# Kernel optimization log

Measured on AMD Instinct MI355X. Metric: run time of the kernel, lower is better.

The kernel has to match this reference:

```python
import jax, jax.numpy as jnp
import numpy as np

N_NODES = 100000
N_EDGES = 3200000  # avg degree 32
IN_FEATS = 512
N_HIDDEN = 128
N_CLASSES = 64
K = 10  # n_layers of gated APPNP propagation


def setup_inputs() -> dict:
    key = jax.random.key(0)
    ks = jax.random.split(key, 6)
    features = jax.random.normal(ks[0], (N_NODES, IN_FEATS), dtype=jnp.float32)
    W1 = jax.random.normal(ks[1], (IN_FEATS, N_HIDDEN), dtype=jnp.float32) * (1.0 / np.sqrt(IN_FEATS))
    b1 = jnp.zeros((N_HIDDEN,), jnp.float32)
    W2 = jax.random.normal(ks[2], (N_HIDDEN, N_CLASSES), dtype=jnp.float32) * (1.0 / np.sqrt(N_HIDDEN))
    b2 = jnp.zeros((N_CLASSES,), jnp.float32)
    init_weight_y = jax.random.normal(ks[3], (IN_FEATS, N_CLASSES), dtype=jnp.float32) * (1.0 / np.sqrt(IN_FEATS))
    edge_index = jax.random.randint(ks[4], (2, N_EDGES), 0, N_NODES, dtype=jnp.int32)
    return {
        "features": features, "W1": W1, "b1": b1, "W2": W2, "b2": b2,
        "init_weight_y": init_weight_y, "edge_index": edge_index,
    }


def reference(features, W1, b1, W2, b2, init_weight_y, edge_index):
    # Eval-mode forward: feat/edge dropout are identity.
    src, dst = edge_index[0], edge_index[1]
    n = features.shape[0]
    # Symmetric GCN normalization D^{-1/2} A D^{-1/2} from in-degrees.
    deg = jax.ops.segment_sum(jnp.ones(src.shape, features.dtype), dst, num_segments=n)
    norm = jax.lax.rsqrt(jnp.clip(deg, 1.0))
    ew = (norm[src] * norm[dst])[:, None]  # [E,1] edge weights

    def spmm(x):  # A_hat @ x via gather-multiply-scatter
        return jax.ops.segment_sum(x[src] * ew, dst, num_segments=n)

    # feature transform: dropout(identity) -> linear -> relu
    h = jax.nn.relu(features @ W1 + b1)                      # [N,H]
    logits = jax.nn.softmax(features @ init_weight_y, axis=1)  # [N,C]
    # project predictions before propagation (APPNP propagates class scores)
    h0 = h @ W2 + b2                                         # [N,C]

    def step(carry, _):
        hc, lg = carry
        agg_lg = spmm(lg)                                    # neighbor soft labels
        # gate: per-node agreement between own and aggregated soft labels
        z = jax.nn.sigmoid(jnp.sum(lg * agg_lg, axis=1, keepdims=True))  # [N,1]
        h_new = z * spmm(hc) + (1.0 - z) * h0                # gated APPNP hop
        return (h_new, agg_lg), None

    (h_out, _), _ = jax.lax.scan(step, (h0, logits), None, length=K)
    return h_out
```

## Files before the change

### kernel.cpp

```cpp
#include <hip/hip_runtime.h>

typedef __attribute__((ext_vector_type(8))) short bf16x8;
typedef __attribute__((ext_vector_type(4))) short bf16x4;
typedef __attribute__((ext_vector_type(4))) float f32x4;
typedef __attribute__((ext_vector_type(4))) unsigned int u32x4;

__device__ __forceinline__ unsigned short f2bf(float f) {
  unsigned int u = __float_as_uint(f);
  u += 0x7fffu + ((u >> 16) & 1u);
  return (unsigned short)(u >> 16);
}
__device__ __forceinline__ float bflo(unsigned int w) { return __uint_as_float(w << 16); }
__device__ __forceinline__ float bfhi(unsigned int w) { return __uint_as_float(w & 0xffff0000u); }

__device__ __forceinline__ short* ldsp(short* base, int row, int rowbytes, int colshort) {
  int off = row * rowbytes + colshort * 2;
  off ^= ((row & 7) << 4);
  return (short*)((char*)base + off);
}

#define CHUNK 8192
#define NBMAX 512

__global__ __launch_bounds__(256) void k_bhist(const int* __restrict__ ei, int E, int NB,
                                               int* __restrict__ gcnt, int* __restrict__ wghist) {
  __shared__ int h[NBMAX];
  for (int t = threadIdx.x; t < NB; t += 256) h[t] = 0;
  __syncthreads();
  int base = blockIdx.x * CHUNK;
#pragma unroll
  for (int i = 0; i < CHUNK / 256; ++i) {
    int e = base + i * 256 + threadIdx.x;
    if (e < E) atomicAdd(&h[ei[E + e] >> 8], 1);
  }
  __syncthreads();
  for (int t = threadIdx.x; t < NB; t += 256) {
    int c = h[t];
    wghist[blockIdx.x * NBMAX + t] = c;
    if (c) atomicAdd(&gcnt[t], c);
  }
}

__global__ void k_bscan(const int* __restrict__ gcnt, int* __restrict__ bbase,
                        int* __restrict__ gcur, int* __restrict__ offs, int NB, int N) {
  __shared__ int sm[512];
  int t = threadIdx.x;
  int v = (t < NB) ? gcnt[t] : 0;
  sm[t] = v;
  __syncthreads();
  for (int o = 1; o < 512; o <<= 1) {
    int x = (t >= o) ? sm[t - o] : 0;
    __syncthreads();
    sm[t] += x;
    __syncthreads();
  }
  if (t < NB) { int e = sm[t] - v; bbase[t] = e; gcur[t] = e; }
  if (t == 511) { bbase[NB] = sm[511]; offs[N] = sm[511]; }
}

__global__ __launch_bounds__(256) void k_bucket(const int* __restrict__ ei,
                                                const int* __restrict__ wghist,
                                                int* __restrict__ gcur,
                                                int2* __restrict__ bpairs, int E, int NB) {
  __shared__ int lbase[NBMAX];
  __shared__ int lcur[NBMAX];
  for (int t = threadIdx.x; t < NB; t += 256) {
    int c = wghist[blockIdx.x * NBMAX + t];
    lbase[t] = c ? atomicAdd(&gcur[t], c) : 0;
    lcur[t] = 0;
  }
  __syncthreads();
  int base = blockIdx.x * CHUNK;
#pragma unroll
  for (int i = 0; i < CHUNK / 256; ++i) {
    int e = base + i * 256 + threadIdx.x;
    if (e < E) {
      int s = ei[e], d = ei[E + e];
      int b = d >> 8;
      int p = lbase[b] + atomicAdd(&lcur[b], 1);
      bpairs[p] = make_int2(s, d);
    }
  }
}

__global__ __launch_bounds__(256) void k_csr(const int2* __restrict__ bpairs,
                                             const int* __restrict__ bbase,
                                             int* __restrict__ offs, float* __restrict__ nrm,
                                             int* __restrict__ csr_src,
                                             int* __restrict__ gslots, int N) {
  __shared__ int hist[256];
  __shared__ int scan[256];
  __shared__ int cur[256];
  const int t = threadIdx.x;
  const int b = blockIdx.x;
  const int d0 = b << 8;
  const int nn = min(256, N - d0);
  const int base = bbase[b], end = bbase[b + 1];
  hist[t] = 0;
  __syncthreads();
  for (int e = base + t; e < end; e += 256) atomicAdd(&hist[bpairs[e].y - d0], 1);
  __syncthreads();
  int myc = hist[t];
  scan[t] = myc;
  __syncthreads();
  for (int o = 1; o < 256; o <<= 1) {
    int x = (t >= o) ? scan[t - o] : 0;
    __syncthreads();
    scan[t] += x;
    __syncthreads();
  }
  int excl = scan[t] - myc;
  if (t < nn) {
    offs[d0 + t] = base + excl;
    nrm[d0 + t] = rsqrtf(fmaxf((float)myc, 1.f));
  }
  if (t < 64) {
    int w0 = hist[4 * t + 0], w1 = hist[4 * t + 1];
    int w2 = hist[4 * t + 2], w3 = hist[4 * t + 3];
    gslots[b * 64 + t] = 4 * max(max(w0, w1), max(w2, w3));
  }
  cur[t] = excl;
  __syncthreads();
  for (int e = base + t; e < end; e += 256) {
    int2 pr = bpairs[e];
    int pos = atomicAdd(&cur[pr.y - d0], 1);
    csr_src[base + pos] = pr.x;
  }
}

__global__ void k_scan1(const int* __restrict__ in, int* __restrict__ out,
                        int* __restrict__ bsum, int n) {
  __shared__ int sm[1024];
  int t = threadIdx.x;
  int gid = blockIdx.x * 1024 + t;
  int v = (gid < n) ? in[gid] : 0;
  sm[t] = v;
  __syncthreads();
  for (int off = 1; off < 1024; off <<= 1) {
    int x = (t >= off) ? sm[t - off] : 0;
    __syncthreads();
    sm[t] += x;
    __syncthreads();
  }
  if (gid < n) out[gid] = sm[t] - v;
  if (t == 1023) bsum[blockIdx.x] = sm[1023];
}

__global__ void k_scan2(int* __restrict__ bsum, int nb) {
  __shared__ int sm[128];
  int t = threadIdx.x;
  int v = (t < nb) ? bsum[t] : 0;
  sm[t] = v;
  __syncthreads();
  for (int o = 1; o < 128; o <<= 1) {
    int x = (t >= o) ? sm[t - o] : 0;
    __syncthreads();
    sm[t] += x;
    __syncthreads();
  }
  if (t < nb) bsum[t] = sm[t] - v;
  if (t == 127) bsum[nb] = sm[127];
}

__global__ void k_scan3(int* __restrict__ out, const int* __restrict__ bsum, int n) {
  int gid = blockIdx.x * 1024 + threadIdx.x;
  if (gid < n) out[gid] += bsum[blockIdx.x];
  if (gid == 0) out[n] = bsum[gridDim.x];
}

__global__ __launch_bounds__(64) void k_ell(
    const int* __restrict__ offs, const int* __restrict__ csr_src,
    const int* __restrict__ gof, unsigned* __restrict__ pidx,
    unsigned int* __restrict__ pkA, unsigned int* __restrict__ pkB, int N) {
  int g = blockIdx.x;
  int t = threadIdx.x;
  if (g == 0) {
    pkA[(size_t)N * 64 + t] = 0;
    pkB[(size_t)N * 64 + t] = 0;
  }
  int base = gof[g];
  int slots = gof[g + 1] - base;
  int o[4], d[4];
#pragma unroll
  for (int s = 0; s < 4; ++s) {
    int nd_ = g * 4 + s;
    o[s] = (nd_ < N) ? offs[nd_] : 0;
    d[s] = (nd_ < N) ? (offs[nd_ + 1] - o[s]) : 0;
  }
  unsigned zoff = (unsigned)N << 8;
  for (int j = t; j < slots; j += 64) {
    int i = j >> 2, s = j & 3;
    pidx[base + j] = (i < d[s]) ? ((unsigned)csr_src[o[s] + i] << 8) : zoff;
  }
}

__global__ void k_wprep(const float* __restrict__ W1, const float* __restrict__ Wy,
                        unsigned short* __restrict__ Wt) {
  int k = blockIdx.x, j = threadIdx.x;
  float v = (j < 128) ? W1[k * 128 + j] : Wy[k * 64 + (j - 128)];
  Wt[j * 512 + k] = f2bf(v);
}
__global__ void k_wprep2(const float* __restrict__ W2, unsigned short* __restrict__ Wt2) {
  int k = blockIdx.x, j = threadIdx.x;
  Wt2[j * 128 + k] = f2bf(W2[k * 64 + j]);
}

__global__ __launch_bounds__(256) void k_transform(
    const unsigned short* __restrict__ Wt, const unsigned short* __restrict__ Wt2,
    const float* __restrict__ X, const float* __restrict__ b1, const float* __restrict__ b2,
    const float* __restrict__ nrm,
    unsigned int* __restrict__ pk0, unsigned short* __restrict__ h0b, int n)
{
  __shared__ short Xs[128 * 32];
  __shared__ short Ws[192 * 32];
  __shared__ short Hs[128 * 128];
  __shared__ short W2s[64 * 128];

  const int tid = threadIdx.x;
  const int w = tid >> 6;
  const int lane = tid & 63;
  const int c = lane & 15;
  const int g = lane >> 4;
  const int m0 = blockIdx.x * 128;

#pragma unroll
  for (int i = 0; i < 4; ++i) {
    int cc = tid + i * 256;
    int j2 = cc >> 4, k8 = (cc & 15) * 8;
    bf16x8 v = *(const bf16x8*)&Wt2[j2 * 128 + k8];
    *(bf16x8*)ldsp(W2s, j2, 256, k8) = v;
  }

  f32x4 zero4 = {0.f, 0.f, 0.f, 0.f};
  f32x4 acc[2][12];
#pragma unroll
  for (int mi = 0; mi < 2; ++mi)
#pragma unroll
    for (int i = 0; i < 12; ++i) acc[mi][i] = zero4;

  const int xr = tid >> 1;
  const int xc = (tid & 1) * 16;
  const int xrow = m0 + xr;

  for (int kk = 0; kk < 512; kk += 32) {
    float4 f[4];
    if (xrow < n) {
      const float4* p = (const float4*)(X + (size_t)xrow * 512 + kk + xc);
      f[0] = p[0]; f[1] = p[1]; f[2] = p[2]; f[3] = p[3];
    } else {
      float4 z = {0.f, 0.f, 0.f, 0.f};
      f[0] = z; f[1] = z; f[2] = z; f[3] = z;
    }
    bf16x8 lo, hi;
    {
      const float* fp = (const float*)f;
#pragma unroll
      for (int q = 0; q < 8; ++q) { lo[q] = (short)f2bf(fp[q]); hi[q] = (short)f2bf(fp[8 + q]); }
    }
    *(bf16x8*)ldsp(Xs, xr, 64, xc) = lo;
    *(bf16x8*)ldsp(Xs, xr, 64, xc + 8) = hi;
#pragma unroll
    for (int i = 0; i < 3; ++i) {
      int cc = tid + i * 256;
      int j = cc >> 2, k8 = (cc & 3) * 8;
      bf16x8 v = *(const bf16x8*)&Wt[j * 512 + kk + k8];
      *(bf16x8*)ldsp(Ws, j, 64, k8) = v;
    }
    __syncthreads();
    bf16x8 bx0 = *(const bf16x8*)ldsp(Xs, w * 32 + c, 64, g * 8);
    bf16x8 bx1 = *(const bf16x8*)ldsp(Xs, w * 32 + 16 + c, 64, g * 8);
#pragma unroll
    for (int jt = 0; jt < 12; ++jt) {
      bf16x8 aw = *(const bf16x8*)ldsp(Ws, jt * 16 + c, 64, g * 8);
      acc[0][jt] = __builtin_amdgcn_mfma_f32_16x16x32_bf16(aw, bx0, acc[0][jt], 0, 0, 0);
      acc[1][jt] = __builtin_amdgcn_mfma_f32_16x16x32_bf16(aw, bx1, acc[1][jt], 0, 0, 0);
    }
    __syncthreads();
  }

  float lv[2][16];
  float inv_[2];
#pragma unroll
  for (int mi = 0; mi < 2; ++mi) {
    int m = w * 32 + mi * 16 + c;
#pragma unroll
    for (int jt = 0; jt < 8; ++jt) {
      int jb = jt * 16 + g * 4;
      bf16x4 hv;
#pragma unroll
      for (int q = 0; q < 4; ++q) {
        float hvf = fmaxf(acc[mi][jt][q] + b1[jb + q], 0.f);
        hv[q] = (short)f2bf(hvf);
      }
      *(bf16x4*)ldsp(Hs, m, 256, jb) = hv;
    }
    float mx = -3.4e38f;
#pragma unroll
    for (int t = 0; t < 4; ++t)
#pragma unroll
      for (int q = 0; q < 4; ++q) {
        float vv = acc[mi][8 + t][q];
        lv[mi][t * 4 + q] = vv;
        mx = fmaxf(mx, vv);
      }
    mx = fmaxf(mx, __shfl_xor(mx, 16, 64));
    mx = fmaxf(mx, __shfl_xor(mx, 32, 64));
    float sum = 0.f;
#pragma unroll
    for (int i = 0; i < 16; ++i) { lv[mi][i] = __expf(lv[mi][i] - mx); sum += lv[mi][i]; }
    sum += __shfl_xor(sum, 16, 64);
    sum += __shfl_xor(sum, 32, 64);
    inv_[mi] = 1.f / sum;
  }
  __syncthreads();

  f32x4 acc2[2][4];
#pragma unroll
  for (int mi = 0; mi < 2; ++mi)
#pragma unroll
    for (int i = 0; i < 4; ++i) acc2[mi][i] = zero4;
#pragma unroll
  for (int kk2 = 0; kk2 < 4; ++kk2) {
    bf16x8 bh0 = *(const bf16x8*)ldsp(Hs, w * 32 + c, 256, kk2 * 32 + g * 8);
    bf16x8 bh1 = *(const bf16x8*)ldsp(Hs, w * 32 + 16 + c, 256, kk2 * 32 + g * 8);
#pragma unroll
    for (int j2t = 0; j2t < 4; ++j2t) {
      bf16x8 a2 = *(const bf16x8*)ldsp(W2s, j2t * 16 + c, 256, kk2 * 32 + g * 8);
      acc2[0][j2t] = __builtin_amdgcn_mfma_f32_16x16x32_bf16(a2, bh0, acc2[0][j2t], 0, 0, 0);
      acc2[1][j2t] = __builtin_amdgcn_mfma_f32_16x16x32_bf16(a2, bh1, acc2[1][j2t], 0, 0, 0);
    }
  }

#pragma unroll
  for (int mi = 0; mi < 2; ++mi) {
    int m = w * 32 + mi * 16 + c;
    int grow = m0 + m;
    if (grow < n) {
      float nd = nrm[grow];
#pragma unroll
      for (int t = 0; t < 4; ++t) {
        int cb = t * 16 + g * 4;
        u32x4 pkv;
        bf16x4 hb;
#pragma unroll
        for (int q = 0; q < 4; ++q) {
          float lg  = lv[mi][t * 4 + q] * inv_[mi];
          float h0v = acc2[mi][t][q] + b2[cb + q];
          hb[q]  = (short)f2bf(h0v);
          pkv[q] = ((unsigned)f2bf(nd * h0v) << 16) | (unsigned)f2bf(nd * lg);
        }
        *(u32x4*)(pk0 + (size_t)grow * 64 + cb) = pkv;
        *(bf16x4*)(h0b + (size_t)grow * 64 + cb) = hb;
      }
    }
  }
}

__global__ __launch_bounds__(256) void k_prop(
    const int* __restrict__ gof, const unsigned* __restrict__ pidx,
    const unsigned int* __restrict__ pk_in, unsigned int* __restrict__ pk_out,
    const unsigned short* __restrict__ h0b, const float* __restrict__ nrm,
    float* __restrict__ final_out, int n, int ng, int last)
{
  const int lane = threadIdx.x & 63;
  const int g = blockIdx.x * 4 + (threadIdx.x >> 6);
  if (g >= ng) return;
  const int sub = lane >> 4;
  const int cq  = lane & 15;
  const int node = g * 4 + sub;
  const int beg = gof[g];
  const int w = (gof[g + 1] - beg) >> 2;
  const char* pkc = (const char*)pk_in;
  const unsigned* ib = pidx + beg + sub;
  const int coff = cq << 4;

  float aL[4] = {0.f, 0.f, 0.f, 0.f}, aH[4] = {0.f, 0.f, 0.f, 0.f};
  float bL[4] = {0.f, 0.f, 0.f, 0.f}, bH[4] = {0.f, 0.f, 0.f, 0.f};
  int i = 0;
  for (; i + 2 <= w; i += 2) {
    unsigned r0 = ib[4 * i];
    unsigned r1 = ib[4 * i + 4];
    u32x4 w0 = *(const u32x4*)(pkc + r0 + coff);
    u32x4 w1 = *(const u32x4*)(pkc + r1 + coff);
#pragma unroll
    for (int q = 0; q < 4; ++q) {
      aL[q] += bflo(w0[q]); aH[q] += bfhi(w0[q]);
      bL[q] += bflo(w1[q]); bH[q] += bfhi(w1[q]);
    }
  }
  if (i < w) {
    unsigned r0 = ib[4 * i];
    u32x4 w0 = *(const u32x4*)(pkc + r0 + coff);
#pragma unroll
    for (int q = 0; q < 4; ++q) { aL[q] += bflo(w0[q]); aH[q] += bfhi(w0[q]); }
  }
#pragma unroll
  for (int q = 0; q < 4; ++q) { aL[q] += bL[q]; aH[q] += bH[q]; }

  if (node >= n) return;
  u32x4 own = *(const u32x4*)(pkc + (node << 8) + coff);
  float p = 0.f;
#pragma unroll
  for (int q = 0; q < 4; ++q) p += bflo(own[q]) * aL[q];
  p += __shfl_xor(p, 1, 64);
  p += __shfl_xor(p, 2, 64);
  p += __shfl_xor(p, 4, 64);
  p += __shfl_xor(p, 8, 64);
  float z = 1.f / (1.f + __expf(-p));
  float nd = nrm[node];
  bf16x4 h0v = *(const bf16x4*)(h0b + (size_t)node * 64 + cq * 4);

  if (last) {
    float4 o;
    float* op = &o.x;
#pragma unroll
    for (int q = 0; q < 4; ++q) {
      float h0f = __uint_as_float(((unsigned)(unsigned short)h0v[q]) << 16);
      op[q] = z * nd * aH[q] + (1.f - z) * h0f;
    }
    *(float4*)(final_out + (size_t)node * 64 + cq * 4) = o;
  } else {
    u32x4 pkv;
    float nn2 = nd * nd;
#pragma unroll
    for (int q = 0; q < 4; ++q) {
      float h0f = __uint_as_float(((unsigned)(unsigned short)h0v[q]) << 16);
      float hn = z * nd * aH[q] + (1.f - z) * h0f;
      pkv[q] = ((unsigned)f2bf(nd * hn) << 16) | (unsigned)f2bf(nn2 * aL[q]);
    }
    *(u32x4*)((char*)pk_out + (node << 8) + coff) = pkv;
  }
}

extern "C" void kernel_launch(void* const* d_in, const int* in_sizes, int n_in,
                              void* d_out, int out_size, void* d_ws, size_t ws_size,
                              hipStream_t stream) {
  (void)n_in; (void)out_size; (void)ws_size;
  const float* X  = (const float*)d_in[0];
  const float* W1 = (const float*)d_in[1];
  const float* b1 = (const float*)d_in[2];
  const float* W2 = (const float*)d_in[3];
  const float* b2 = (const float*)d_in[4];
  const float* Wy = (const float*)d_in[5];
  const int*   ei = (const int*)d_in[6];
  const int N = in_sizes[0] / 512;
  const int E = in_sizes[6] / 2;
  const int NB = (N + 255) >> 8;
  const int NG = NB * 64;
  const int NWG = (E + CHUNK - 1) / CHUNK;

  char* p = (char*)d_ws;
  auto alloc = [&](size_t bytes) -> char* {
    char* r = p; p += (bytes + 255) & ~(size_t)255; return r;
  };
  int*            gcnt    = (int*)  alloc(NBMAX * 4);
  int*            bbase   = (int*)  alloc((NBMAX + 1) * 4);
  int*            gcur    = (int*)  alloc(NBMAX * 4);
  int*            wghist  = (int*)  alloc((size_t)NWG * NBMAX * 4);
  int*            offs    = (int*)  alloc((size_t)(N + 1) * 4);
  float*          nrm     = (float*)alloc((size_t)N * 4);
  int*            csr_src = (int*)  alloc((size_t)E * 4);
  int*            gslots  = (int*)  alloc((size_t)(NG + 1) * 4);
  int*            gof     = (int*)  alloc((size_t)(NG + 1) * 4);
  int*            sbsum   = (int*)  alloc(1024);
  unsigned*       pidx    = (unsigned*)alloc((size_t)2 * E * 4);
  unsigned short* Wt      = (unsigned short*)alloc(192 * 512 * 2);
  unsigned short* Wt2     = (unsigned short*)alloc(64 * 128 * 2);
  size_t pkbytes = (size_t)(N + 1) * 64 * 4;
  size_t bpbytes = (size_t)E * 8;
  char*           shared0 = alloc(pkbytes > bpbytes ? pkbytes : bpbytes);
  int2*           bpairs  = (int2*)shared0;
  unsigned int*   pkA     = (unsigned int*)shared0;
  unsigned int*   pkB     = (unsigned int*)alloc(pkbytes);
  unsigned short* h0b     = (unsigned short*)alloc((size_t)N * 64 * 2);

  hipMemsetAsync(gcnt, 0, NBMAX * 4, stream);

  k_wprep<<<512, 192, 0, stream>>>(W1, Wy, Wt);
  k_wprep2<<<128, 64, 0, stream>>>(W2, Wt2);
  k_bhist<<<NWG, 256, 0, stream>>>(ei, E, NB, gcnt, wghist);
  k_bscan<<<1, 512, 0, stream>>>(gcnt, bbase, gcur, offs, NB, N);
  k_bucket<<<NWG, 256, 0, stream>>>(ei, wghist, gcur, bpairs, E, NB);
  k_csr<<<NB, 256, 0, stream>>>(bpairs, bbase, offs, nrm, csr_src, gslots, N);
  int nb2 = (NG + 1023) / 1024;
  k_scan1<<<nb2, 1024, 0, stream>>>(gslots, gof, sbsum, NG);
  k_scan2<<<1, 128, 0, stream>>>(sbsum, nb2);
  k_scan3<<<nb2, 1024, 0, stream>>>(gof, sbsum, NG);
  k_ell<<<NG, 64, 0, stream>>>(offs, csr_src, gof, pidx, pkA, pkB, N);
  k_transform<<<(N + 127) / 128, 256, 0, stream>>>(Wt, Wt2, X, b1, b2, nrm, pkA, h0b, N);

  for (int k = 0; k < 10; ++k) {
    const unsigned int* in  = (k & 1) ? pkB : pkA;
    unsigned int*       out = (k & 1) ? pkA : pkB;
    k_prop<<<(NG + 3) / 4, 256, 0, stream>>>(gof, pidx, in, out, h0b, nrm,
                                             (float*)d_out, N, NG, (k == 9) ? 1 : 0);
  }
}
```

Measured before the change: 1.334 ms.

## Sort neighbor lists per node, unroll gather by four, hoist own-node loads

The ELL build step now copies each node's neighbor list (up to a degree cap) into shared memory and insertion-sorts it, so gathers in propagation visit source rows in ascending address order for better cache locality. The propagation gather loop is unrolled to four outstanding 16-byte loads per iteration instead of two, adding memory-level parallelism. The node's own packed row, norm and h0 loads are hoisted ahead of the gather loop so their latency overlaps it. The cost is a serial per-thread insertion sort in setup and higher register pressure in the propagation kernel.

```diff
diff --git a/kernel.cpp b/kernel.cpp
--- a/kernel.cpp
+++ b/kernel.cpp
@@ -21,6 +21,7 @@
 
 #define CHUNK 8192
 #define NBMAX 512
+#define DCAP 96
 
 __global__ __launch_bounds__(256) void k_bhist(const int* __restrict__ ei, int E, int NB,
                                                int* __restrict__ gcnt, int* __restrict__ wghist) {
@@ -172,6 +173,7 @@
     const int* __restrict__ offs, const int* __restrict__ csr_src,
     const int* __restrict__ gof, unsigned* __restrict__ pidx,
     unsigned int* __restrict__ pkA, unsigned int* __restrict__ pkB, int N) {
+  __shared__ int buf[4][DCAP];
   int g = blockIdx.x;
   int t = threadIdx.x;
   if (g == 0) {
@@ -187,10 +189,27 @@
     o[s] = (nd_ < N) ? offs[nd_] : 0;
     d[s] = (nd_ < N) ? (offs[nd_ + 1] - o[s]) : 0;
   }
+#pragma unroll
+  for (int s = 0; s < 4; ++s)
+    if (d[s] <= DCAP)
+      for (int i = t; i < d[s]; i += 64) buf[s][i] = csr_src[o[s] + i];
+  __syncthreads();
+  if (t < 4 && d[t] <= DCAP) {
+    int dd = d[t];
+    for (int i = 1; i < dd; ++i) {
+      int key = buf[t][i];
+      int j = i - 1;
+      while (j >= 0 && buf[t][j] > key) { buf[t][j + 1] = buf[t][j]; --j; }
+      buf[t][j + 1] = key;
+    }
+  }
+  __syncthreads();
   unsigned zoff = (unsigned)N << 8;
   for (int j = t; j < slots; j += 64) {
     int i = j >> 2, s = j & 3;
-    pidx[base + j] = (i < d[s]) ? ((unsigned)csr_src[o[s] + i] << 8) : zoff;
+    unsigned v = zoff;
+    if (i < d[s]) v = (unsigned)((d[s] <= DCAP) ? buf[s][i] : csr_src[o[s] + i]) << 8;
+    pidx[base + j] = v;
   }
 }
 
@@ -374,21 +393,32 @@
   const unsigned* ib = pidx + beg + sub;
   const int coff = cq << 4;
 
+  const int nodeC = (node < n) ? node : 0;
+  u32x4 own = *(const u32x4*)(pkc + ((size_t)nodeC << 8) + coff);
+  float nd = nrm[nodeC];
+  bf16x4 h0v = *(const bf16x4*)(h0b + (size_t)nodeC * 64 + cq * 4);
+
   float aL[4] = {0.f, 0.f, 0.f, 0.f}, aH[4] = {0.f, 0.f, 0.f, 0.f};
   float bL[4] = {0.f, 0.f, 0.f, 0.f}, bH[4] = {0.f, 0.f, 0.f, 0.f};
   int i = 0;
-  for (; i + 2 <= w; i += 2) {
+  for (; i + 4 <= w; i += 4) {
     unsigned r0 = ib[4 * i];
     unsigned r1 = ib[4 * i + 4];
+    unsigned r2 = ib[4 * i + 8];
+    unsigned r3 = ib[4 * i + 12];
     u32x4 w0 = *(const u32x4*)(pkc + r0 + coff);
     u32x4 w1 = *(const u32x4*)(pkc + r1 + coff);
+    u32x4 w2 = *(const u32x4*)(pkc + r2 + coff);
+    u32x4 w3 = *(const u32x4*)(pkc + r3 + coff);
 #pragma unroll
     for (int q = 0; q < 4; ++q) {
-      aL[q] += bflo(w0[q]); aH[q] += bfhi(w0[q]);
-      bL[q] += bflo(w1[q]); bH[q] += bfhi(w1[q]);
-    }
-  }
-  if (i < w) {
+      aL[q] += bflo(w0[q]) + bflo(w2[q]);
+      aH[q] += bfhi(w0[q]) + bfhi(w2[q]);
+      bL[q] += bflo(w1[q]) + bflo(w3[q]);
+      bH[q] += bfhi(w1[q]) + bfhi(w3[q]);
+    }
+  }
+  for (; i < w; ++i) {
     unsigned r0 = ib[4 * i];
     u32x4 w0 = *(const u32x4*)(pkc + r0 + coff);
 #pragma unroll
@@ -398,7 +428,6 @@
   for (int q = 0; q < 4; ++q) { aL[q] += bL[q]; aH[q] += bH[q]; }
 
   if (node >= n) return;
-  u32x4 own = *(const u32x4*)(pkc + (node << 8) + coff);
   float p = 0.f;
 #pragma unroll
   for (int q = 0; q < 4; ++q) p += bflo(own[q]) * aL[q];
@@ -407,8 +436,6 @@
   p += __shfl_xor(p, 4, 64);
   p += __shfl_xor(p, 8, 64);
   float z = 1.f / (1.f + __expf(-p));
-  float nd = nrm[node];
-  bf16x4 h0v = *(const bf16x4*)(h0b + (size_t)node * 64 + cq * 4);
 
   if (last) {
     float4 o;
@@ -428,7 +455,7 @@
       float hn = z * nd * aH[q] + (1.f - z) * h0f;
       pkv[q] = ((unsigned)f2bf(nd * hn) << 16) | (unsigned)f2bf(nn2 * aL[q]);
     }
-    *(u32x4*)((char*)pk_out + (node << 8) + coff) = pkv;
+    *(u32x4*)((char*)pk_out + ((size_t)node << 8) + coff) = pkv;
   }
 }
 
```

Result: slower. 1.625 ms (+21.9%).
